# Kernel optimization log

Measured on AMD Instinct MI355X. Metric: run time of the kernel, lower is better.

## Reference

```python
import jax, jax.numpy as jnp
import numpy as np

MARGIN = 0.2  # matches init_kwargs; margin > 0 -> relu hinge branch

N_PARTS, NUM_CLASSES, K_PER_CLASS, D_FEAT = 64, 32, 16, 256


def setup_inputs() -> dict:
    key = jax.random.key(0)
    m = NUM_CLASSES * K_PER_CLASS  # 512
    feature = jax.random.normal(key, (N_PARTS, m, D_FEAT), dtype=jnp.float32)
    # Structured P x K labels: masked_select(...).view(n, m, -1, 1) in the
    # original requires exactly K positives per anchor, so labels must be
    # K samples per class (identical across the part dimension).
    label = jnp.tile(jnp.repeat(jnp.arange(NUM_CLASSES, dtype=jnp.int64), K_PER_CLASS)[None, :], (N_PARTS, 1))
    return {"feature": feature, "label": label, "num_pos": K_PER_CLASS}


def _batch_euc_dist(x):
    # x: [n, m, d] -> dist: [n, m, m]
    x2 = jnp.sum(x * x, axis=2)  # [n, m]
    d2 = x2[:, :, None] + x2[:, None, :] - 2.0 * jnp.einsum('nid,njd->nij', x, x)
    return jnp.sqrt(jax.nn.relu(d2))


def reference(feature, label, num_pos):
    n, m, d = feature.shape
    dist = _batch_euc_dist(feature)  # [n, m, m]
    same = label[:, :, None] == label[:, None, :]  # [n, m, m] bool
    # masked_select preserves flat (row-major) order, so per anchor the
    # selected positives/negatives appear in increasing index order ->
    # stable argsort on the mask reproduces it exactly.
    pos_idx = jnp.argsort(jnp.where(same, 0, 1), axis=-1)[..., :num_pos]        # [n, m, k]
    neg_idx = jnp.argsort(jnp.where(same, 1, 0), axis=-1)[..., :m - num_pos]    # [n, m, m-k]
    hp = jnp.take_along_axis(dist, pos_idx, axis=-1)[:, :, :, None]   # [n, m, k, 1]
    hn = jnp.take_along_axis(dist, neg_idx, axis=-1)[:, :, None, :]   # [n, m, 1, m-k]
    # margin > 0 -> relu hinge (heter/hard/part mining disabled by init flags)
    loss = jax.nn.relu(MARGIN + hp - hn).reshape(n, -1)               # [n, m*k*(m-k)]
    nonzero_num = jnp.sum(loss != 0, axis=1).astype(loss.dtype)       # [n]
    loss_mean = jnp.where(nonzero_num == 0, 0.0,
                          jnp.sum(loss, axis=1) / jnp.maximum(nonzero_num, 1.0))
    return loss_mean.mean(), nonzero_num.mean()
```

## Files before the change

### kernel.cpp

```cpp
#include <hip/hip_runtime.h>
#include <math.h>


#define MARGIN 0.2f
constexpr int NP = 64;
constexpr int M = 512;
constexpr int D = 256;
constexpr int SDS = 20;

typedef __attribute__((ext_vector_type(8))) short bf16x8;
typedef __attribute__((ext_vector_type(4))) float f32x4;
typedef __attribute__((address_space(1))) const unsigned int as1_uint;
typedef __attribute__((address_space(3))) unsigned int as3_uint;

__device__ __forceinline__ unsigned f2bf(float x) {
  unsigned b = __float_as_uint(x);
  return (b + 0x7FFFu + ((b >> 16) & 1u)) >> 16;
}
__device__ __forceinline__ uint4 pack8u(float4 v0, float4 v1) {
  uint4 p;
  p.x = f2bf(v0.x) | (f2bf(v0.y) << 16);
  p.y = f2bf(v0.z) | (f2bf(v0.w) << 16);
  p.z = f2bf(v1.x) | (f2bf(v1.y) << 16);
  p.w = f2bf(v1.z) | (f2bf(v1.w) << 16);
  return p;
}
__device__ __forceinline__ float sq8(float4 v0, float4 v1) {
  return v0.x * v0.x + v0.y * v0.y + v0.z * v0.z + v0.w * v0.w +
         v1.x * v1.x + v1.y * v1.y + v1.z * v1.z + v1.w * v1.w;
}

__global__ __launch_bounds__(256) void convert_kernel(
    const float* __restrict__ feat, unsigned short* __restrict__ fb,
    float* __restrict__ x2g) {
  const int t = threadIdx.x;
  const int R = blockIdx.x * 8 + (t >> 5);
  const int c = t & 31;
  const int r = R & 63;
  const float* src = feat + (size_t)R * D + c * 8;
  float4 v0 = ((const float4*)src)[0], v1 = ((const float4*)src)[1];
  *(uint4*)&fb[((size_t)R * 32 + (c ^ (r & 7))) * 8] = pack8u(v0, v1);
  float ss = sq8(v0, v1);
  ss += __shfl_xor(ss, 16, 32);
  ss += __shfl_xor(ss, 8, 32);
  ss += __shfl_xor(ss, 4, 32);
  ss += __shfl_xor(ss, 2, 32);
  ss += __shfl_xor(ss, 1, 32);
  if (c == 0) x2g[R] = ss;
}

__global__ __launch_bounds__(256, 2) void triplet_kernel(
    const unsigned short* __restrict__ fb, const float* __restrict__ x2g,
    float* __restrict__ psum, float* __restrict__ pcnt) {
  __shared__ unsigned short Bs[64 * 32 * 8];
  __shared__ float sortd[64 * SDS];
  __shared__ float sumt[64 * SDS];
  __shared__ float x2s[2][64];
  __shared__ float reds[4], redc[4];

  const int p = blockIdx.x;
  const int diag = blockIdx.y;
  const int h = blockIdx.z;
  const int i0 = diag * 64;
  const int t = threadIdx.x;
  const int w = t >> 6, L = t & 63;
  const int tx = L & 15, quad = L >> 4;
  const int tx7 = tx & 7;
  const float* x2p = x2g + (size_t)p * M;

  auto dma_tile = [&](int j0) {
    const char* gsrc = (const char*)fb + ((size_t)p * M + j0) * 512;
    char* lbase = (char*)Bs + (t >> 6) * 1024;
#pragma unroll
    for (int i = 0; i < 8; i++)
      __builtin_amdgcn_global_load_lds((as1_uint*)(gsrc + i * 4096 + t * 16),
                                       (as3_uint*)(lbase + i * 4096), 16, 0, 0);
  };

  dma_tile(i0);
  if (t < 64) x2s[0][t] = x2p[i0 + t];

  const size_t Ra = (size_t)p * M + i0 + w * 16 + tx;
  bf16x8 af[8];
#pragma unroll
  for (int kc = 0; kc < 2; kc++)
#pragma unroll
    for (int ks = 0; ks < 4; ks++) {
      const int ca = kc * 16 + ks * 4 + quad;
      af[kc * 4 + ks] = *(const bf16x8*)&fb[(Ra * 32 + (ca ^ tx7)) * 8];
    }
  float x2i[4];
#pragma unroll
  for (int r = 0; r < 4; r++) x2i[r] = x2p[i0 + w * 16 + quad * 4 + r];

  f32x4 srt[4][4];
  float hsum = 0.f;
  int hcnt = 0;

  const int ntiles = 4 + h;
  for (int ti = 0; ti < ntiles; ti++) {
    const int cur = ti & 1;
    __syncthreads();

    f32x4 acc[4];
#pragma unroll
    for (int f = 0; f < 4; f++) acc[f] = (f32x4){0.f, 0.f, 0.f, 0.f};
#pragma unroll
    for (int kc = 0; kc < 2; kc++)
#pragma unroll
      for (int ks = 0; ks < 4; ks++) {
        const bf16x8 a = af[kc * 4 + ks];
        const int cb = kc * 16 + ks * 4 + quad;
#pragma unroll
        for (int f = 0; f < 4; f++) {
          const int rowb = f * 16 + tx;
          bf16x8 b = *(bf16x8*)&Bs[(rowb * 32 + (cb ^ tx7)) * 8];
          acc[f] =
              __builtin_amdgcn_mfma_f32_16x16x32_bf16(a, b, acc[f], 0, 0, 0);
        }
      }

    __syncthreads();

    const int nti = ti + 1;
    const bool havenext = nti < ntiles;
    const int nj0 = havenext ? (((diag + nti + h * 3) & 7) * 64) : 0;
    if (ti != 0 && havenext) {
      dma_tile(nj0);
      if (t < 64) x2s[nti & 1][t] = x2p[nj0 + t];
    }

    if (ti == 0) {
      const float xj = x2s[0][w * 16 + tx];
#pragma unroll
      for (int r = 0; r < 4; r++) {
        float d2 = x2i[r] + xj - 2.f * acc[w][r];
        sortd[(w * 16 + quad * 4 + r) * SDS + tx] =
            MARGIN + sqrtf(fmaxf(d2, 0.f));
      }
      __syncthreads();
      if (t < 64) {
        float v[16];
#pragma unroll
        for (int q4 = 0; q4 < 4; q4++) {
          f32x4 vv = *(f32x4*)&sortd[t * SDS + q4 * 4];
          v[q4 * 4 + 0] = vv.x; v[q4 * 4 + 1] = vv.y;
          v[q4 * 4 + 2] = vv.z; v[q4 * 4 + 3] = vv.w;
        }
#pragma unroll
        for (int k = 2; k <= 16; k <<= 1)
#pragma unroll
          for (int j = k >> 1; j > 0; j >>= 1)
#pragma unroll
            for (int i = 0; i < 16; i++) {
              const int l = i ^ j;
              if (l > i) {
                const bool asc = ((i & k) == 0);
                if (asc ? (v[i] > v[l]) : (v[i] < v[l])) {
                  float tmp = v[i]; v[i] = v[l]; v[l] = tmp;
                }
              }
            }
#pragma unroll
        for (int q4 = 0; q4 < 4; q4++)
          *(f32x4*)&sortd[t * SDS + q4 * 4] =
              (f32x4){v[q4 * 4], v[q4 * 4 + 1], v[q4 * 4 + 2], v[q4 * 4 + 3]};
        float run = 0.f;
        sumt[t * SDS + 0] = 0.f;
#pragma unroll
        for (int c = 1; c <= 16; c++) {
          run += v[16 - c];
          sumt[t * SDS + c] = run;
        }
      }
      __syncthreads();
#pragma unroll
      for (int r = 0; r < 4; r++)
#pragma unroll
        for (int q4 = 0; q4 < 4; q4++)
          srt[r][q4] = *(f32x4*)&sortd[(w * 16 + quad * 4 + r) * SDS + q4 * 4];

      if (havenext) {
        dma_tile(nj0);
        if (t < 64) x2s[nti & 1][t] = x2p[nj0 + t];
      }

      if (h == 0) {
#pragma unroll
        for (int f = 0; f < 4; f++) {
          if (f == w) continue;
          const float xj2 = x2s[0][f * 16 + tx];
#pragma unroll
          for (int r = 0; r < 4; r++) {
            const float dn = sqrtf(fmaxf(x2i[r] + xj2 - 2.f * acc[f][r], 0.f));
            int c = 0;
#define CMP(sv) c += ((sv) > dn) ? 1 : 0;
            CMP(srt[r][0].x) CMP(srt[r][0].y) CMP(srt[r][0].z) CMP(srt[r][0].w)
            CMP(srt[r][1].x) CMP(srt[r][1].y) CMP(srt[r][1].z) CMP(srt[r][1].w)
            CMP(srt[r][2].x) CMP(srt[r][2].y) CMP(srt[r][2].z) CMP(srt[r][2].w)
            CMP(srt[r][3].x) CMP(srt[r][3].y) CMP(srt[r][3].z) CMP(srt[r][3].w)
#undef CMP
            hsum += sumt[(w * 16 + quad * 4 + r) * SDS + c];
            hsum = fmaf(-(float)c, dn, hsum);
            hcnt += c;
          }
        }
      }
    } else {
#pragma unroll
      for (int f = 0; f < 4; f++) {
        const float xj = x2s[cur][f * 16 + tx];
#pragma unroll
        for (int r = 0; r < 4; r++) {
          const float dn = sqrtf(fmaxf(x2i[r] + xj - 2.f * acc[f][r], 0.f));
          int c = 0;
#define CMP(sv) c += ((sv) > dn) ? 1 : 0;
          CMP(srt[r][0].x) CMP(srt[r][0].y) CMP(srt[r][0].z) CMP(srt[r][0].w)
          CMP(srt[r][1].x) CMP(srt[r][1].y) CMP(srt[r][1].z) CMP(srt[r][1].w)
          CMP(srt[r][2].x) CMP(srt[r][2].y) CMP(srt[r][2].z) CMP(srt[r][2].w)
          CMP(srt[r][3].x) CMP(srt[r][3].y) CMP(srt[r][3].z) CMP(srt[r][3].w)
#undef CMP
          hsum += sumt[(w * 16 + quad * 4 + r) * SDS + c];
          hsum = fmaf(-(float)c, dn, hsum);
          hcnt += c;
        }
      }
    }
  }

  float cf = (float)hcnt;
  for (int off = 32; off > 0; off >>= 1) {
    hsum += __shfl_down(hsum, off, 64);
    cf += __shfl_down(cf, off, 64);
  }
  if (L == 0) { reds[w] = hsum; redc[w] = cf; }
  __syncthreads();
  if (t == 0) {
    psum[p * 16 + diag * 2 + h] = reds[0] + reds[1] + reds[2] + reds[3];
    pcnt[p * 16 + diag * 2 + h] = redc[0] + redc[1] + redc[2] + redc[3];
  }
}

__global__ __launch_bounds__(64) void finalize_kernel(
    const float* __restrict__ psum, const float* __restrict__ pcnt,
    float* __restrict__ out) {
  const int p = threadIdx.x;
  float s = 0.f, c = 0.f;
#pragma unroll
  for (int i = 0; i < 16; i++) {
    s += psum[p * 16 + i];
    c += pcnt[p * 16 + i];
  }
  float lm = (c == 0.f) ? 0.f : s / fmaxf(c, 1.f);
  float ctot = c;
  for (int off = 32; off > 0; off >>= 1) {
    lm += __shfl_down(lm, off, 64);
    ctot += __shfl_down(ctot, off, 64);
  }
  if (p == 0) {
    out[0] = lm / 64.f;
    out[1] = ctot / 64.f;
  }
}

extern "C" void kernel_launch(void* const* d_in, const int* in_sizes, int n_in,
                              void* d_out, int out_size, void* d_ws,
                              size_t ws_size, hipStream_t stream) {
  const float* feat = (const float*)d_in[0];
  float* ws = (float*)d_ws;
  float* psum = ws;
  float* pcnt = ws + 1024;
  float* x2g = ws + 2048;
  unsigned short* fb = (unsigned short*)(ws + 2048 + 32768);
  float* out = (float*)d_out;

  convert_kernel<<<(NP * M) / 8, 256, 0, stream>>>(feat, fb, x2g);
  dim3 grid(NP, 8, 2);
  triplet_kernel<<<grid, 256, 0, stream>>>(fb, x2g, psum, pcnt);
  finalize_kernel<<<1, 64, 0, stream>>>(psum, pcnt, out);
}
```

Baseline: 122.9 us.

## Split column tiles across 8 waves per block instead of splitting j-range over blocks

Replaces the two-block split of each row strip's column tiles (h=0/1, 4 and 5 tiles) with a single 512-thread block of 8 waves. Each wave pair shares a 16-row strip and each wave computes half of every 64-column tile, so every block walks all 8 tiles. This halves the grid and removes the uneven per-block tile counts, and each shared tile load now feeds twice as many waves. In exchange each block runs more serial tiles with more barrier participants, and the requested 4 blocks per CU of 512 threads may limit registers.

```diff
diff --git a/kernel.cpp b/kernel.cpp
--- a/kernel.cpp
+++ b/kernel.cpp
@@ -49,38 +49,39 @@
   if (c == 0) x2g[R] = ss;
 }
 
-__global__ __launch_bounds__(256, 2) void triplet_kernel(
+__global__ __launch_bounds__(512, 4) void triplet_kernel(
     const unsigned short* __restrict__ fb, const float* __restrict__ x2g,
     float* __restrict__ psum, float* __restrict__ pcnt) {
   __shared__ unsigned short Bs[64 * 32 * 8];
   __shared__ float sortd[64 * SDS];
   __shared__ float sumt[64 * SDS];
   __shared__ float x2s[2][64];
-  __shared__ float reds[4], redc[4];
+  __shared__ float reds[8], redc[8];
 
   const int p = blockIdx.x;
   const int diag = blockIdx.y;
-  const int h = blockIdx.z;
   const int i0 = diag * 64;
   const int t = threadIdx.x;
   const int w = t >> 6, L = t & 63;
+  const int rw = w & 3;
+  const int fh = w >> 1 >> 1;
   const int tx = L & 15, quad = L >> 4;
   const int tx7 = tx & 7;
   const float* x2p = x2g + (size_t)p * M;
 
   auto dma_tile = [&](int j0) {
     const char* gsrc = (const char*)fb + ((size_t)p * M + j0) * 512;
-    char* lbase = (char*)Bs + (t >> 6) * 1024;
-#pragma unroll
-    for (int i = 0; i < 8; i++)
-      __builtin_amdgcn_global_load_lds((as1_uint*)(gsrc + i * 4096 + t * 16),
-                                       (as3_uint*)(lbase + i * 4096), 16, 0, 0);
+    char* lbase = (char*)Bs + w * 1024;
+#pragma unroll
+    for (int i = 0; i < 4; i++)
+      __builtin_amdgcn_global_load_lds((as1_uint*)(gsrc + i * 8192 + t * 16),
+                                       (as3_uint*)(lbase + i * 8192), 16, 0, 0);
   };
 
   dma_tile(i0);
   if (t < 64) x2s[0][t] = x2p[i0 + t];
 
-  const size_t Ra = (size_t)p * M + i0 + w * 16 + tx;
+  const size_t Ra = (size_t)p * M + i0 + rw * 16 + tx;
   bf16x8 af[8];
 #pragma unroll
   for (int kc = 0; kc < 2; kc++)
@@ -91,20 +92,20 @@
     }
   float x2i[4];
 #pragma unroll
-  for (int r = 0; r < 4; r++) x2i[r] = x2p[i0 + w * 16 + quad * 4 + r];
+  for (int r = 0; r < 4; r++) x2i[r] = x2p[i0 + rw * 16 + quad * 4 + r];
 
   f32x4 srt[4][4];
   float hsum = 0.f;
   int hcnt = 0;
 
-  const int ntiles = 4 + h;
-  for (int ti = 0; ti < ntiles; ti++) {
+  for (int ti = 0; ti < 8; ti++) {
     const int cur = ti & 1;
+    const int j0 = ((diag + ti) & 7) * 64;
     __syncthreads();
 
-    f32x4 acc[4];
-#pragma unroll
-    for (int f = 0; f < 4; f++) acc[f] = (f32x4){0.f, 0.f, 0.f, 0.f};
+    f32x4 acc[2];
+    acc[0] = (f32x4){0.f, 0.f, 0.f, 0.f};
+    acc[1] = (f32x4){0.f, 0.f, 0.f, 0.f};
 #pragma unroll
     for (int kc = 0; kc < 2; kc++)
 #pragma unroll
@@ -112,31 +113,33 @@
         const bf16x8 a = af[kc * 4 + ks];
         const int cb = kc * 16 + ks * 4 + quad;
 #pragma unroll
-        for (int f = 0; f < 4; f++) {
-          const int rowb = f * 16 + tx;
+        for (int ff = 0; ff < 2; ff++) {
+          const int rowb = (fh * 2 + ff) * 16 + tx;
           bf16x8 b = *(bf16x8*)&Bs[(rowb * 32 + (cb ^ tx7)) * 8];
-          acc[f] =
-              __builtin_amdgcn_mfma_f32_16x16x32_bf16(a, b, acc[f], 0, 0, 0);
+          acc[ff] =
+              __builtin_amdgcn_mfma_f32_16x16x32_bf16(a, b, acc[ff], 0, 0, 0);
         }
       }
 
     __syncthreads();
 
-    const int nti = ti + 1;
-    const bool havenext = nti < ntiles;
-    const int nj0 = havenext ? (((diag + nti + h * 3) & 7) * 64) : 0;
+    const bool havenext = ti < 7;
+    const int nj0 = ((diag + ti + 1) & 7) * 64;
     if (ti != 0 && havenext) {
       dma_tile(nj0);
-      if (t < 64) x2s[nti & 1][t] = x2p[nj0 + t];
+      if (t < 64) x2s[(ti + 1) & 1][t] = x2p[nj0 + t];
     }
 
     if (ti == 0) {
-      const float xj = x2s[0][w * 16 + tx];
-#pragma unroll
-      for (int r = 0; r < 4; r++) {
-        float d2 = x2i[r] + xj - 2.f * acc[w][r];
-        sortd[(w * 16 + quad * 4 + r) * SDS + tx] =
-            MARGIN + sqrtf(fmaxf(d2, 0.f));
+      if ((rw >> 1) == fh) {
+        const int ff = rw & 1;
+        const float xj = x2s[0][rw * 16 + tx];
+#pragma unroll
+        for (int r = 0; r < 4; r++) {
+          float d2 = x2i[r] + xj - 2.f * acc[ff][r];
+          sortd[(rw * 16 + quad * 4 + r) * SDS + tx] =
+              MARGIN + sqrtf(fmaxf(d2, 0.f));
+        }
       }
       __syncthreads();
       if (t < 64) {
@@ -178,52 +181,32 @@
       for (int r = 0; r < 4; r++)
 #pragma unroll
         for (int q4 = 0; q4 < 4; q4++)
-          srt[r][q4] = *(f32x4*)&sortd[(w * 16 + quad * 4 + r) * SDS + q4 * 4];
+          srt[r][q4] = *(f32x4*)&sortd[(rw * 16 + quad * 4 + r) * SDS + q4 * 4];
 
       if (havenext) {
         dma_tile(nj0);
-        if (t < 64) x2s[nti & 1][t] = x2p[nj0 + t];
-      }
-
-      if (h == 0) {
-#pragma unroll
-        for (int f = 0; f < 4; f++) {
-          if (f == w) continue;
-          const float xj2 = x2s[0][f * 16 + tx];
-#pragma unroll
-          for (int r = 0; r < 4; r++) {
-            const float dn = sqrtf(fmaxf(x2i[r] + xj2 - 2.f * acc[f][r], 0.f));
-            int c = 0;
+        if (t < 64) x2s[1][t] = x2p[nj0 + t];
+      }
+    }
+
+#pragma unroll
+    for (int ff = 0; ff < 2; ff++) {
+      const int f = fh * 2 + ff;
+      if (ti == 0 && f == rw) continue;
+      const float xj = x2s[cur][f * 16 + tx];
+#pragma unroll
+      for (int r = 0; r < 4; r++) {
+        const float dn = sqrtf(fmaxf(x2i[r] + xj - 2.f * acc[ff][r], 0.f));
+        int c = 0;
 #define CMP(sv) c += ((sv) > dn) ? 1 : 0;
-            CMP(srt[r][0].x) CMP(srt[r][0].y) CMP(srt[r][0].z) CMP(srt[r][0].w)
-            CMP(srt[r][1].x) CMP(srt[r][1].y) CMP(srt[r][1].z) CMP(srt[r][1].w)
-            CMP(srt[r][2].x) CMP(srt[r][2].y) CMP(srt[r][2].z) CMP(srt[r][2].w)
-            CMP(srt[r][3].x) CMP(srt[r][3].y) CMP(srt[r][3].z) CMP(srt[r][3].w)
+        CMP(srt[r][0].x) CMP(srt[r][0].y) CMP(srt[r][0].z) CMP(srt[r][0].w)
+        CMP(srt[r][1].x) CMP(srt[r][1].y) CMP(srt[r][1].z) CMP(srt[r][1].w)
+        CMP(srt[r][2].x) CMP(srt[r][2].y) CMP(srt[r][2].z) CMP(srt[r][2].w)
+        CMP(srt[r][3].x) CMP(srt[r][3].y) CMP(srt[r][3].z) CMP(srt[r][3].w)
 #undef CMP
-            hsum += sumt[(w * 16 + quad * 4 + r) * SDS + c];
-            hsum = fmaf(-(float)c, dn, hsum);
-            hcnt += c;
-          }
-        }
-      }
-    } else {
-#pragma unroll
-      for (int f = 0; f < 4; f++) {
-        const float xj = x2s[cur][f * 16 + tx];
-#pragma unroll
-        for (int r = 0; r < 4; r++) {
-          const float dn = sqrtf(fmaxf(x2i[r] + xj - 2.f * acc[f][r], 0.f));
-          int c = 0;
-#define CMP(sv) c += ((sv) > dn) ? 1 : 0;
-          CMP(srt[r][0].x) CMP(srt[r][0].y) CMP(srt[r][0].z) CMP(srt[r][0].w)
-          CMP(srt[r][1].x) CMP(srt[r][1].y) CMP(srt[r][1].z) CMP(srt[r][1].w)
-          CMP(srt[r][2].x) CMP(srt[r][2].y) CMP(srt[r][2].z) CMP(srt[r][2].w)
-          CMP(srt[r][3].x) CMP(srt[r][3].y) CMP(srt[r][3].z) CMP(srt[r][3].w)
-#undef CMP
-          hsum += sumt[(w * 16 + quad * 4 + r) * SDS + c];
-          hsum = fmaf(-(float)c, dn, hsum);
-          hcnt += c;
-        }
+        hsum += sumt[(rw * 16 + quad * 4 + r) * SDS + c];
+        hsum = fmaf(-(float)c, dn, hsum);
+        hcnt += c;
       }
     }
   }
@@ -236,8 +219,11 @@
   if (L == 0) { reds[w] = hsum; redc[w] = cf; }
   __syncthreads();
   if (t == 0) {
-    psum[p * 16 + diag * 2 + h] = reds[0] + reds[1] + reds[2] + reds[3];
-    pcnt[p * 16 + diag * 2 + h] = redc[0] + redc[1] + redc[2] + redc[3];
+    float bs = 0.f, bc = 0.f;
+#pragma unroll
+    for (int i = 0; i < 8; i++) { bs += reds[i]; bc += redc[i]; }
+    psum[p * 8 + diag] = bs;
+    pcnt[p * 8 + diag] = bc;
   }
 }
 
@@ -247,9 +233,9 @@
   const int p = threadIdx.x;
   float s = 0.f, c = 0.f;
 #pragma unroll
-  for (int i = 0; i < 16; i++) {
-    s += psum[p * 16 + i];
-    c += pcnt[p * 16 + i];
+  for (int i = 0; i < 8; i++) {
+    s += psum[p * 8 + i];
+    c += pcnt[p * 8 + i];
   }
   float lm = (c == 0.f) ? 0.f : s / fmaxf(c, 1.f);
   float ctot = c;
@@ -269,13 +255,13 @@
   const float* feat = (const float*)d_in[0];
   float* ws = (float*)d_ws;
   float* psum = ws;
-  float* pcnt = ws + 1024;
-  float* x2g = ws + 2048;
-  unsigned short* fb = (unsigned short*)(ws + 2048 + 32768);
+  float* pcnt = ws + 512;
+  float* x2g = ws + 1024;
+  unsigned short* fb = (unsigned short*)(ws + 1024 + 32768);
   float* out = (float*)d_out;
 
   convert_kernel<<<(NP * M) / 8, 256, 0, stream>>>(feat, fb, x2g);
-  dim3 grid(NP, 8, 2);
-  triplet_kernel<<<grid, 256, 0, stream>>>(fb, x2g, psum, pcnt);
+  dim3 grid(NP, 8);
+  triplet_kernel<<<grid, 512, 0, stream>>>(fb, x2g, psum, pcnt);
   finalize_kernel<<<1, 64, 0, stream>>>(psum, pcnt, out);
 }
```

After: 132.7 us. 8.0% more time.
